# Kernel tuning notes

Hardware: AMD Instinct MI355X
Metric: run time of the kernel (lower is better)

The kernel has to match this reference:

```python
import jax, jax.numpy as jnp
import numpy as np
from jax.scipy.stats import norm as jnorm

B, S, D, H, E, K, FF = 8, 256, 1024, 16, 4, 2, 4096
HD = D // H
NOISE_EPS = 0.01
LOSS_COEF = 0.01
EPS_FILL = float(np.finfo(float).eps)


def _ln(x, g, b):
    m = x.mean(-1, keepdims=True)
    v = x.var(-1, keepdims=True)
    return (x - m) * jax.lax.rsqrt(v + 1e-5) * g + b


def setup_inputs() -> dict:
    key = jax.random.key(0)
    ks = jax.random.split(key, 16)
    r = lambda i, shape, s=1.0: jax.random.normal(ks[i], shape, dtype=jnp.float32) * s
    return {
        "x": r(0, (B, S, D)),
        "e_outputs": r(1, (B, 64, D)),            # unused (is_lm=True) but part of signature
        "noise": r(2, (B, E)),                     # the randn_like(clean_logits) draw
        "w_gate": r(3, (D, E), 0.02),
        "w_noise": r(4, (D, E), 0.02),
        "Wq": r(5, (E, D, D), 0.02),
        "Wk": r(6, (E, D, D), 0.02),
        "Wv": r(7, (E, D, D), 0.02),
        "Wo": r(8, (E, D, D), 0.02),
        "W1": r(9, (E, D, FF), 0.02),
        "b1": jnp.zeros((E, FF), jnp.float32),
        "W2": r(10, (E, FF, D), 0.02),
        "b2": jnp.zeros((E, D), jnp.float32),
        "g1": jnp.ones((E, D), jnp.float32),
        "be1": jnp.zeros((E, D), jnp.float32),
        "g2": jnp.ones((E, D), jnp.float32),
        "be2": jnp.zeros((E, D), jnp.float32),
        "trg_mask": jnp.tril(jnp.ones((S, S), dtype=bool))[None, None],  # causal [1,1,S,S]
        "src_mask": jnp.ones((1, 1, 1, 64), dtype=bool),                 # unused (is_lm=True)
    }


def _cv_squared(v):
    # torch .var() is unbiased (ddof=1)
    return v.var(ddof=1) / (v.mean() ** 2 + 1e-10)


def reference(x, e_outputs, noise, w_gate, w_noise, Wq, Wk, Wv, Wo, W1, b1, W2, b2,
              g1, be1, g2, be2, trg_mask, src_mask):
    b, s, d = x.shape
    # ---- noisy top-k gating (per sample, on the sequence-sum) ----
    xs = x.sum(axis=1)                                   # [B, D]
    clean = xs @ w_gate                                  # [B, E]
    raw_noise = xs @ w_noise                             # [B, E]
    stddev = jax.nn.softplus(raw_noise) + NOISE_EPS      # train=True -> *1.0
    noisy = clean + noise * stddev                       # logits
    top_logits, top_idx = jax.lax.top_k(noisy, K + 1)    # [B, K+1]
    topk_gates = jax.nn.softmax(top_logits[:, :K], axis=1)
    gates = jnp.zeros_like(noisy).at[jnp.arange(b)[:, None], top_idx[:, :K]].set(topk_gates)
    # load: prob each expert's clean logit lands in the noisy top-k
    thr_in = top_logits[:, K:K + 1]                      # (k+1)-th noisy value
    thr_out = top_logits[:, K - 1:K]                     # k-th noisy value
    is_in = noisy > thr_in
    prob = jnp.where(is_in,
                     jnorm.cdf((clean - thr_in) / stddev),
                     jnorm.cdf((clean - thr_out) / stddev))
    load = prob.sum(0)                                   # [E]
    importance = gates.sum(0)                            # [E]
    loss = (_cv_squared(importance) + _cv_squared(load)) * LOSS_COEF

    # ---- experts: standard decoder layer (self-attn + FFN), is_lm -> no cross-attn ----
    neg = jnp.asarray(-1e9, x.dtype)
    scale = 1.0 / np.sqrt(HD)

    def expert(p):
        wq, wk, wv, wo, w1, bb1, w2, bb2, gg1, bbe1, gg2, bbe2 = p
        q = (x @ wq).reshape(b, s, H, HD)
        k_ = (x @ wk).reshape(b, s, H, HD)
        v = (x @ wv).reshape(b, s, H, HD)
        scores = jnp.einsum('bqhd,bkhd->bhqk', q, k_) * scale
        scores = jnp.where(trg_mask, scores, neg)
        attn = jax.nn.softmax(scores, axis=-1)
        o = jnp.einsum('bhqk,bkhd->bqhd', attn, v).reshape(b, s, d) @ wo
        h = _ln(x + o, gg1, bbe1)
        ff = jax.nn.relu(h @ w1 + bb1) @ w2 + bb2
        return _ln(h + ff, gg2, bbe2)

    outs = jax.vmap(expert)((Wq, Wk, Wv, Wo, W1, b1, W2, b2, g1, be1, g2, be2))  # [E,B,S,D]

    # ---- combine: scatter-add of gate-weighted expert outputs (dense equivalent) ----
    y = jnp.einsum('be,ebsd->bsd', gates, outs)
    y = jnp.where(y == 0, jnp.asarray(EPS_FILL, y.dtype), y)
    return y, loss
```

## Files before the change

### kernel.cpp

```cpp
#include <hip/hip_runtime.h>
#include <hip/hip_bf16.h>

typedef __bf16 bf16;
typedef __attribute__((ext_vector_type(4))) __bf16 bf16x4;
typedef __attribute__((ext_vector_type(8))) __bf16 bf16x8;
typedef __attribute__((ext_vector_type(4))) float floatx4;

constexpr int CB = 8, CS = 256, CD = 1024, CH = 16, CE = 4, CFF = 4096, CHD = 64;
constexpr long long DD  = 1048576;
constexpr long long DFF = 4194304;
constexpr long long BSD = 2097152;
constexpr long long PSD = 4194304;

constexpr size_t OFF_PART = 0;
constexpr size_t OFF_CLEAN= 262144;
constexpr size_t OFF_RAW  = 262272;
constexpr size_t OFF_GATES= 262400;
constexpr size_t OFF_EACT = 262528;
constexpr size_t OFF_PBE  = 262592;
constexpr size_t OFF_BP   = 262656;
constexpr size_t OFF_XBF  = 263168;
constexpr size_t OFF_WT   = OFF_XBF + (size_t)BSD*2;
constexpr size_t OFF_W1T  = OFF_WT  + (size_t)16*DD*2;
constexpr size_t OFF_W2T  = OFF_W1T + (size_t)4*DFF*2;
constexpr size_t OFF_QKV  = OFF_W2T + (size_t)4*DFF*2;
constexpr size_t OFF_AO   = OFF_QKV + (size_t)3*PSD*2;
constexpr size_t OFF_F1   = OFF_QKV;
constexpr size_t OFF_PB   = OFF_AO  + (size_t)PSD*2;
constexpr size_t OFF_VT   = OFF_PB;
constexpr size_t OFF_H    = OFF_PB  + (size_t)2*PSD*4;
constexpr size_t OFF_HBF  = OFF_H   + (size_t)PSD*4;

__global__ __launch_bounds__(256)
void wtrans_cvt(const float* __restrict__ Wq, const float* __restrict__ Wk,
                const float* __restrict__ Wv, const float* __restrict__ Wo,
                const float* __restrict__ W1, const float* __restrict__ W2,
                bf16* __restrict__ wT, bf16* __restrict__ w1T, bf16* __restrict__ w2T,
                const float* __restrict__ x, bf16* __restrict__ xbf, float* __restrict__ part) {
  int zb = blockIdx.x;
  if (zb >= 3072) {
    int blk = zb - 3072;
    int b = blk >> 3, ch = blk & 7;
    int t = threadIdx.x;
    float s0 = 0.f, s1 = 0.f, s2 = 0.f, s3 = 0.f;
    long long base4 = ((long long)(b*CS + ch*32))*CD / 4;
#pragma unroll 4
    for (int r = 0; r < 32; ++r) {
      long long i4 = base4 + (long long)r*(CD/4) + t;
      float4 v = ((const float4*)x)[i4];
      bf16x4 o; o[0] = (bf16)v.x; o[1] = (bf16)v.y; o[2] = (bf16)v.z; o[3] = (bf16)v.w;
      ((bf16x4*)xbf)[i4] = o;
      s0 += v.x; s1 += v.y; s2 += v.z; s3 += v.w;
    }
    float4 sv; sv.x = s0; sv.y = s1; sv.z = s2; sv.w = s3;
    ((float4*)(part + (long long)blk*CD))[t] = sv;
    return;
  }
  int w = threadIdx.x >> 6;
  const float* src; bf16* d; int rows, cols, btk, btn;
  if (zb < 1024) {
    int m = zb >> 6, bt = zb & 63; int e = m >> 2; int which = m & 3;
    src = ((which == 0) ? Wq : (which == 1) ? Wk : (which == 2) ? Wv : Wo) + (long long)e*DD;
    d = wT + (long long)m*DD; rows = 1024; cols = 1024;
    btk = bt >> 3; btn = bt & 7;
  } else if (zb < 2048) {
    int z2 = zb - 1024; int e = z2 >> 8; int bt = z2 & 255;
    src = W1 + (long long)e*DFF; d = w1T + (long long)e*DFF;
    rows = 1024; cols = 4096; btk = bt >> 5; btn = bt & 31;
  } else {
    int z3 = zb - 2048; int e = z3 >> 8; int bt = z3 & 255;
    src = W2 + (long long)e*DFF; d = w2T + (long long)e*DFF;
    rows = 4096; cols = 1024; btk = bt >> 3; btn = bt & 7;
  }
  int tk = btk*2 + (w & 1);
  int tn = btn*2 + (w >> 1);
  int lane = threadIdx.x & 63;
  int ln = lane >> 3, lk = lane & 7;
  int k0 = tk*64, n0 = tn*64;
  const float* s = src + (long long)(k0 + lk*8)*cols + n0 + ln*8;
  floatx4 f[8][2];
#pragma unroll
  for (int j = 0; j < 8; ++j) {
    f[j][0] = __builtin_nontemporal_load((const floatx4*)(s + (long long)j*cols));
    f[j][1] = __builtin_nontemporal_load((const floatx4*)(s + (long long)j*cols + 4));
  }
  bf16* dp = d + (long long)(n0 + ln*8)*rows + k0 + lk*8;
#pragma unroll
  for (int jn = 0; jn < 8; ++jn) {
    bf16x8 o;
#pragma unroll
    for (int jk = 0; jk < 8; ++jk) {
      o[jk] = (bf16)f[jk][jn >> 2][jn & 3];
    }
    *(bf16x8*)(dp + (long long)jn*rows) = o;
  }
}

__global__ __launch_bounds__(256)
void gate_fused(const float* __restrict__ part, const float* __restrict__ wg,
                const float* __restrict__ wn, const float* __restrict__ noise,
                float* __restrict__ gates, int* __restrict__ eact, int* __restrict__ pairBE,
                int* __restrict__ batchPair, float* __restrict__ loss_out) {
  int t = threadIdx.x;
  float4 wgv[4], wnv[4];
  float xv[CB][4];
#pragma unroll
  for (int k = 0; k < 4; ++k) {
    int d = t + k*256;
    wgv[k] = ((const float4*)wg)[d];
    wnv[k] = ((const float4*)wn)[d];
#pragma unroll
    for (int b = 0; b < CB; ++b) {
      float s = 0.f;
#pragma unroll
      for (int c = 0; c < 8; ++c) s += part[(long long)(b*8 + c)*CD + d];
      xv[b][k] = s;
    }
  }
  __shared__ float red[4][64];
  __shared__ float sCR[64];
  int lane = t & 63, wv = t >> 6;
#pragma unroll
  for (int b = 0; b < CB; ++b) {
#pragma unroll
    for (int e = 0; e < CE; ++e) {
      float s1 = 0.f, s2 = 0.f;
#pragma unroll
      for (int k = 0; k < 4; ++k) {
        const float* g  = (const float*)&wgv[k];
        const float* nn = (const float*)&wnv[k];
        s1 += xv[b][k]*g[e];
        s2 += xv[b][k]*nn[e];
      }
      for (int off = 32; off; off >>= 1) { s1 += __shfl_xor(s1, off); s2 += __shfl_xor(s2, off); }
      if (lane == 0) { red[wv][b*4 + e] = s1; red[wv][32 + b*4 + e] = s2; }
    }
  }
  __syncthreads();
  if (t < 64) sCR[t] = red[0][t] + red[1][t] + red[2][t] + red[3][t];
  __syncthreads();
  if (t != 0) return;
  const float* clean = sCR;
  const float* raw   = sCR + 32;
  float imp[CE] = {0,0,0,0}, load[CE] = {0,0,0,0};
  int act[CE] = {0,0,0,0};
  for (int b = 0; b < CB; ++b) {
    float cl[CE], sd[CE], ny[CE];
    for (int e = 0; e < CE; ++e) {
      cl[e] = clean[b*CE + e];
      float rw = raw[b*CE + e];
      float sp = fmaxf(rw, 0.f) + log1pf(expf(-fabsf(rw)));
      sd[e] = sp + 0.01f;
      ny[e] = cl[e] + noise[b*CE + e]*sd[e];
    }
    int idx[CE] = {0,1,2,3};
    for (int a = 0; a < 3; ++a) {
      int best = a;
      for (int c = a + 1; c < 4; ++c) if (ny[idx[c]] > ny[idx[best]]) best = c;
      int tt = idx[a]; idx[a] = idx[best]; idx[best] = tt;
    }
    float l0 = ny[idx[0]], l1 = ny[idx[1]], l2 = ny[idx[2]];
    float e1 = expf(l1 - l0);
    float g0 = 1.f/(1.f + e1), g1v = e1/(1.f + e1);
    for (int e = 0; e < CE; ++e) gates[b*CE + e] = 0.f;
    gates[b*CE + idx[0]] = g0; gates[b*CE + idx[1]] = g1v;
    imp[idx[0]] += g0; imp[idx[1]] += g1v;
    act[idx[0]] = 1; act[idx[1]] = 1;
    for (int e = 0; e < CE; ++e) {
      bool is_in = ny[e] > l2;
      float thr = is_in ? l2 : l1;
      float zz = (cl[e] - thr) / sd[e];
      load[e] += 0.5f * erfcf(-zz * 0.70710678118654752440f);
    }
  }
  int pe2p[CB][CE];
  int pc = 0;
  for (int e = 0; e < CE; ++e)
    for (int b = 0; b < CB; ++b)
      if (gates[b*CE + e] != 0.f) { pairBE[pc] = b | (e << 8); pe2p[b][e] = pc; ++pc; }
  for (int b = 0; b < CB; ++b) {
    int s = 0;
    for (int e = 0; e < CE; ++e)
      if (gates[b*CE + e] != 0.f) batchPair[2*b + (s++)] = pe2p[b][e];
  }
  float m1 = 0.f, m2 = 0.f;
  for (int e = 0; e < CE; ++e) { m1 += imp[e]; m2 += load[e]; }
  m1 *= 0.25f; m2 *= 0.25f;
  float v1 = 0.f, v2 = 0.f;
  for (int e = 0; e < CE; ++e) { float d1 = imp[e]-m1, d2 = load[e]-m2; v1 += d1*d1; v2 += d2*d2; }
  v1 *= (1.f/3.f); v2 *= (1.f/3.f);
  loss_out[0] = 0.01f * (v1/(m1*m1 + 1e-10f) + v2/(m2*m2 + 1e-10f));
  for (int e = 0; e < CE; ++e) eact[e] = act[e];
}

__global__ __launch_bounds__(256)
void transpose_v(const bf16* __restrict__ qkvC, bf16* __restrict__ vTb) {
  int z = blockIdx.x; int p = z >> 4, h = z & 15;
  int w = threadIdx.x >> 6, lane = threadIdx.x & 63;
  int ln = lane >> 3, lk = lane & 7;
  const bf16* v = qkvC + 2*PSD + ((long long)(p*CS + w*64 + ln*8))*CD + h*CHD + lk*8;
  bf16x8 in[8];
#pragma unroll
  for (int j = 0; j < 8; ++j) in[j] = *(const bf16x8*)(v + (long long)j*CD);
  bf16* vt = vTb + ((long long)(p*CH + h)*CHD + lk*8)*CS + w*64 + ln*8;
#pragma unroll
  for (int dn = 0; dn < 8; ++dn) {
    bf16x8 o;
#pragma unroll
    for (int j = 0; j < 8; ++j) o[j] = in[j][dn];
    *(bf16x8*)(vt + (long long)dn*CS) = o;
  }
}

__device__ __forceinline__ void cp16(const bf16* g, bf16* l) {
  __builtin_amdgcn_global_load_lds((const __attribute__((address_space(1))) void*)g,
                                   (__attribute__((address_space(3))) void*)l, 16, 0, 0);
}

template<int R, int W, int NT>
__device__ __forceinline__ void stageN(const bf16* __restrict__ src, int ld, bf16* dst) {
  constexpr int W8 = W/8;
  int t = threadIdx.x;
  int l = t & 63, wid = t >> 6;
#pragma unroll
  for (int i = 0; i < (R*W8)/NT; ++i) {
    int idb = i*NT + wid*64;
    int id = idb + l;
    int row = id / W8, sl = id % W8;
    int gc = sl ^ (row & 7);
    cp16(src + (long long)row*ld + gc*8, dst + (long long)idb*8);
  }
}

__global__ __launch_bounds__(256)
void attn_fused(const bf16* __restrict__ qkvC, const bf16* __restrict__ vTb,
                bf16* __restrict__ aoC) {
  int h = blockIdx.x, p = blockIdx.y, qt = blockIdx.z;
  const bf16* qp = qkvC + (long long)(p*CS)*CD + h*CHD;
  const bf16* kp = qp + PSD;
  const bf16* vt = vTb + (long long)(p*CH + h)*CHD*CS;
  bf16* aop = aoC + (long long)(p*CS)*CD + h*CHD;

  __shared__ bf16 Ps[64*264];
  __shared__ float smaxL[64*4], ssumL[64*4], Lrow[64];

  int t = threadIdx.x, w = t >> 6, lane = t & 63, lr = lane & 15, quad = lane >> 4;

  floatx4 accs[4][4] = {};
  if (w <= qt) {
#pragma unroll
    for (int kk = 0; kk < 2; ++kk) {
      int c = kk*4 + quad;
      bf16x8 af[4], bfr[4];
#pragma unroll
      for (int i = 0; i < 4; ++i) {
        af[i]  = *(const bf16x8*)(qp + (long long)(qt*64 + i*16 + lr)*CD + c*8);
        bfr[i] = *(const bf16x8*)(kp + (long long)(w*64  + i*16 + lr)*CD + c*8);
      }
#pragma unroll
      for (int i = 0; i < 4; ++i)
#pragma unroll
        for (int j = 0; j < 4; ++j)
          accs[i][j] = __builtin_amdgcn_mfma_f32_16x16x32_bf16(af[i], bfr[j], accs[i][j], 0, 0, 0);
    }
  }
  float rmax[4][4];
#pragma unroll
  for (int i = 0; i < 4; ++i)
#pragma unroll
    for (int r = 0; r < 4; ++r) {
      int qrow = qt*64 + i*16 + quad*4 + r;
      float m = -3.0e38f;
#pragma unroll
      for (int j = 0; j < 4; ++j) {
        int kcol = w*64 + j*16 + lr;
        float s = accs[i][j][r]*0.125f;
        s = (kcol <= qrow) ? s : -3.0e38f;
        accs[i][j][r] = s;
        m = fmaxf(m, s);
      }
      rmax[i][r] = m;
    }
#pragma unroll
  for (int off = 1; off <= 8; off <<= 1)
#pragma unroll
    for (int i = 0; i < 4; ++i)
#pragma unroll
      for (int r = 0; r < 4; ++r) rmax[i][r] = fmaxf(rmax[i][r], __shfl_xor(rmax[i][r], off));
  if (lr == 0)
#pragma unroll
    for (int i = 0; i < 4; ++i)
#pragma unroll
      for (int r = 0; r < 4; ++r) smaxL[(i*16 + quad*4 + r)*4 + w] = rmax[i][r];
  __syncthreads();
  float rsum[4][4];
#pragma unroll
  for (int i = 0; i < 4; ++i)
#pragma unroll
    for (int r = 0; r < 4; ++r) {
      floatx4 mv = *(const floatx4*)&smaxL[(i*16 + quad*4 + r)*4];
      float M = fmaxf(fmaxf(mv[0], mv[1]), fmaxf(mv[2], mv[3]));
      float srow = 0.f;
#pragma unroll
      for (int j = 0; j < 4; ++j) {
        float pp = __expf(accs[i][j][r] - M);
        accs[i][j][r] = pp;
        srow += pp;
      }
      rsum[i][r] = srow;
    }
#pragma unroll
  for (int off = 1; off <= 8; off <<= 1)
#pragma unroll
    for (int i = 0; i < 4; ++i)
#pragma unroll
      for (int r = 0; r < 4; ++r) rsum[i][r] += __shfl_xor(rsum[i][r], off);
  if (lr == 0)
#pragma unroll
    for (int i = 0; i < 4; ++i)
#pragma unroll
      for (int r = 0; r < 4; ++r) ssumL[(i*16 + quad*4 + r)*4 + w] = rsum[i][r];
  __syncthreads();
  if (w == 0 && lr == 0) {
#pragma unroll
    for (int i = 0; i < 4; ++i)
#pragma unroll
      for (int r = 0; r < 4; ++r) {
        int m = i*16 + quad*4 + r;
        floatx4 sv = *(const floatx4*)&ssumL[m*4];
        Lrow[m] = sv[0] + sv[1] + sv[2] + sv[3];
      }
  }
  if (w <= qt) {
#pragma unroll
    for (int i = 0; i < 4; ++i)
#pragma unroll
      for (int j = 0; j < 4; ++j)
#pragma unroll
        for (int r = 0; r < 4; ++r)
          Ps[(i*16 + quad*4 + r)*264 + w*64 + j*16 + lr] = (bf16)accs[i][j][r];
  }
  __syncthreads();
  floatx4 acco[4] = {};
  int ksMax = (qt + 1)*2;
  for (int ks = 0; ks < ksMax; ++ks) {
    int c = ks*4 + quad;
    bf16x8 ap = *(const bf16x8*)(Ps + (w*16 + lr)*264 + c*8);
#pragma unroll
    for (int j = 0; j < 4; ++j) {
      bf16x8 bv = *(const bf16x8*)(vt + (long long)(j*16 + lr)*CS + c*8);
      acco[j] = __builtin_amdgcn_mfma_f32_16x16x32_bf16(ap, bv, acco[j], 0, 0, 0);
    }
  }
#pragma unroll
  for (int r = 0; r < 4; ++r) {
    int orow = w*16 + quad*4 + r;
    float inv = 1.f / Lrow[orow];
#pragma unroll
    for (int j = 0; j < 4; ++j)
      aop[(long long)(qt*64 + orow)*CD + j*16 + lr] = (bf16)(acco[j][r]*inv);
  }
}

__global__ __launch_bounds__(256)
void ln1_kernel(const float* __restrict__ x, const float* __restrict__ PbF,
                const float* __restrict__ gamma, const float* __restrict__ beta,
                float* __restrict__ h, bf16* __restrict__ hbf, const int* __restrict__ pairBE) {
  int row = blockIdx.x;
  int pbe = pairBE[row >> 8]; int pb = pbe & 255, pe = pbe >> 8;
  int t = threadIdx.x;
  float4 a = ((const float4*)(x + ((long long)pb*CS + (row & 255))*CD))[t];
  float4 b = ((const float4*)(PbF + (long long)row*CD))[t];
  float4 c = ((const float4*)(PbF + PSD + (long long)row*CD))[t];
  float v0 = a.x + b.x + c.x, v1 = a.y + b.y + c.y;
  float v2 = a.z + b.z + c.z, v3 = a.w + b.w + c.w;
  float s  = v0 + v1 + v2 + v3;
  float s2 = v0*v0 + v1*v1 + v2*v2 + v3*v3;
  int lane = t & 63, wave = t >> 6;
  for (int off = 32; off; off >>= 1) { s += __shfl_xor(s, off); s2 += __shfl_xor(s2, off); }
  __shared__ float red[8];
  if (lane == 0) { red[wave*2] = s; red[wave*2 + 1] = s2; }
  __syncthreads();
  s  = red[0] + red[2] + red[4] + red[6];
  s2 = red[1] + red[3] + red[5] + red[7];
  float mean = s * (1.f/CD);
  float rstd = rsqrtf(s2*(1.f/CD) - mean*mean + 1e-5f);
  float4 gm = ((const float4*)(gamma + (long long)pe*CD))[t];
  float4 bt = ((const float4*)(beta  + (long long)pe*CD))[t];
  float4 o;
  o.x = (v0 - mean)*rstd*gm.x + bt.x;
  o.y = (v1 - mean)*rstd*gm.y + bt.y;
  o.z = (v2 - mean)*rstd*gm.z + bt.z;
  o.w = (v3 - mean)*rstd*gm.w + bt.w;
  ((float4*)(h + (long long)row*CD))[t] = o;
  bf16x4 ob; ob[0] = (bf16)o.x; ob[1] = (bf16)o.y; ob[2] = (bf16)o.z; ob[3] = (bf16)o.w;
  ((bf16x4*)(hbf + (long long)row*CD))[t] = ob;
}

__global__ __launch_bounds__(256)
void ln2y_kernel(const float* __restrict__ h, const bf16* __restrict__ PbB,
                 const float* __restrict__ gamma, const float* __restrict__ beta,
                 float* __restrict__ y, const float* __restrict__ gates,
                 const int* __restrict__ pairBE, const int* __restrict__ batchPair) {
  int row = blockIdx.x;
  int b = row >> 8, sIdx = row & 255;
  int p0 = batchPair[2*b], p1 = batchPair[2*b + 1];
  int e0 = pairBE[p0] >> 8, e1 = pairBE[p1] >> 8;
  float gv0 = gates[b*CE + e0], gv1 = gates[b*CE + e1];
  long long r0 = (long long)p0*CS + sIdx, r1 = (long long)p1*CS + sIdx;
  int t = threadIdx.x;
  float4 a = ((const float4*)(h + r0*CD))[t];
  float4 c = ((const float4*)(h + r1*CD))[t];
#pragma unroll
  for (int k = 0; k < 4; ++k) {
    bf16x4 pa = ((const bf16x4*)(PbB + (long long)k*PSD + r0*CD))[t];
    bf16x4 pc = ((const bf16x4*)(PbB + (long long)k*PSD + r1*CD))[t];
    a.x += (float)pa[0]; a.y += (float)pa[1]; a.z += (float)pa[2]; a.w += (float)pa[3];
    c.x += (float)pc[0]; c.y += (float)pc[1]; c.z += (float)pc[2]; c.w += (float)pc[3];
  }
  float sA = a.x + a.y + a.z + a.w;
  float sA2 = a.x*a.x + a.y*a.y + a.z*a.z + a.w*a.w;
  float sB = c.x + c.y + c.z + c.w;
  float sB2 = c.x*c.x + c.y*c.y + c.z*c.z + c.w*c.w;
  int lane = t & 63, wave = t >> 6;
  for (int off = 32; off; off >>= 1) {
    sA += __shfl_xor(sA, off); sA2 += __shfl_xor(sA2, off);
    sB += __shfl_xor(sB, off); sB2 += __shfl_xor(sB2, off);
  }
  __shared__ float red[16];
  if (lane == 0) { red[wave*4] = sA; red[wave*4+1] = sA2; red[wave*4+2] = sB; red[wave*4+3] = sB2; }
  __syncthreads();
  sA  = red[0] + red[4] + red[8]  + red[12];
  sA2 = red[1] + red[5] + red[9]  + red[13];
  sB  = red[2] + red[6] + red[10] + red[14];
  sB2 = red[3] + red[7] + red[11] + red[15];
  float mA = sA*(1.f/CD), mB = sB*(1.f/CD);
  float rsA = rsqrtf(sA2*(1.f/CD) - mA*mA + 1e-5f);
  float rsB = rsqrtf(sB2*(1.f/CD) - mB*mB + 1e-5f);
  float4 gm0 = ((const float4*)(gamma + (long long)e0*CD))[t];
  float4 bt0 = ((const float4*)(beta  + (long long)e0*CD))[t];
  float4 gm1 = ((const float4*)(gamma + (long long)e1*CD))[t];
  float4 bt1 = ((const float4*)(beta  + (long long)e1*CD))[t];
  float4 o;
  o.x = gv0*((a.x - mA)*rsA*gm0.x + bt0.x) + gv1*((c.x - mB)*rsB*gm1.x + bt1.x);
  o.y = gv0*((a.y - mA)*rsA*gm0.y + bt0.y) + gv1*((c.y - mB)*rsB*gm1.y + bt1.y);
  o.z = gv0*((a.z - mA)*rsA*gm0.z + bt0.z) + gv1*((c.z - mB)*rsB*gm1.z + bt1.z);
  o.w = gv0*((a.w - mA)*rsA*gm0.w + bt0.w) + gv1*((c.w - mB)*rsB*gm1.w + bt1.w);
  constexpr float EF = 2.2204460492503131e-16f;
  o.x = (o.x == 0.f) ? EF : o.x;  o.y = (o.y == 0.f) ? EF : o.y;
  o.z = (o.z == 0.f) ? EF : o.z;  o.w = (o.w == 0.f) ? EF : o.w;
  ((float4*)(y + (long long)row*CD))[t] = o;
}

enum { EPI_BF16 = 0, EPI_F32 = 1, EPI_BRELU = 2, EPI_BIASBF16 = 3 };

template<int EPI, int KS, bool A_BATCH, int BM>
__global__ __launch_bounds__(512, 2)
void gemm_nt(const bf16* __restrict__ A, const bf16* __restrict__ Bt, void* __restrict__ Cv,
             int K , int lda, int ldb, int ldc,
             long long oBe, long long oBmat, long long oCmat, long long oCk,
             const float* __restrict__ bias, long long biasStride,
             const int* __restrict__ pairBE) {
  constexpr int BN = 256;
  constexpr int NBUF = (BM == 128) ? 3 : 2;
  constexpr int DEPTH = NBUF - 1;
  constexpr int MI = BM / 32;
  int z = blockIdx.z;
  int zk = z % KS, mat = z / KS;
  int gx = gridDim.x;
  int nwg = gx * gridDim.y;
  int lin = blockIdx.x + gx*blockIdx.y;
  int nl  = (lin & 7)*(nwg >> 3) + (lin >> 3);
  int m0 = (nl % gx) * BM, n0 = (nl / gx) * BN;
  int pbe = pairBE[m0 >> 8]; int pb = pbe & 255, pe = pbe >> 8;
  const bf16* Ab = A + (A_BATCH ? ((long long)pb*CS + (m0 & 255))*lda : (long long)m0*lda)
                     + (long long)zk*K;
  const bf16* Bb = Bt + (long long)pe*oBe + (long long)mat*oBmat + (long long)zk*K
                      + (long long)n0*ldb;
  long long coff = (long long)mat*oCmat + (long long)zk*oCk;

  __shared__ bf16 As[NBUF][BM*64];
  __shared__ bf16 Bs[NBUF][BN*64];

  int wave = threadIdx.x >> 6;
  int lane = threadIdx.x & 63;
  int wm = wave >> 2, wn = wave & 3;
  int lr = lane & 15;
  int quad = lane >> 4;

  floatx4 acc[MI][4] = {};

  int nt = K / 64;
#pragma unroll
  for (int d = 0; d < DEPTH; ++d) {
    stageN<BM, 64, 512>(Ab + d*64, lda, As[d]);
    stageN<BN, 64, 512>(Bb + d*64, ldb, Bs[d]);
  }
  int cur = 0, stg = DEPTH;
  for (int t = 0; t < nt; ++t) {
    if (t + DEPTH < nt) {
      stageN<BM, 64, 512>(Ab + (t+DEPTH)*64, lda, As[stg]);
      stageN<BN, 64, 512>(Bb + (t+DEPTH)*64, ldb, Bs[stg]);
      if (++stg == NBUF) stg = 0;
      if constexpr (BM == 128) asm volatile("s_waitcnt vmcnt(12)" ::: "memory");
      else                     asm volatile("s_waitcnt vmcnt(8)"  ::: "memory");
    } else if (t + 1 < nt) {
      if constexpr (BM == 128) asm volatile("s_waitcnt vmcnt(6)"  ::: "memory");
      else                     asm volatile("s_waitcnt vmcnt(0)"  ::: "memory");
    } else {
      asm volatile("s_waitcnt vmcnt(0)" ::: "memory");
    }
    __builtin_amdgcn_s_barrier();
    asm volatile("" ::: "memory");
#pragma unroll
    for (int kk = 0; kk < 2; ++kk) {
      int c = kk*4 + quad;
      bf16x8 af[MI], bfr[4];
#pragma unroll
      for (int i = 0; i < MI; ++i) {
        int m = wm*(BM/2) + i*16 + lr;
        af[i] = *(const bf16x8*)(As[cur] + m*64 + ((c ^ (m & 7))*8));
      }
#pragma unroll
      for (int j = 0; j < 4; ++j) {
        int n = wn*64 + j*16 + lr;
        bfr[j] = *(const bf16x8*)(Bs[cur] + n*64 + ((c ^ (n & 7))*8));
      }
#pragma unroll
      for (int i = 0; i < MI; ++i)
#pragma unroll
        for (int j = 0; j < 4; ++j)
          acc[i][j] = __builtin_amdgcn_mfma_f32_16x16x32_bf16(af[i], bfr[j], acc[i][j], 0, 0, 0);
    }
    if (++cur == NBUF) cur = 0;
    __builtin_amdgcn_s_barrier();
    asm volatile("" ::: "memory");
  }

#pragma unroll
  for (int j = 0; j < 4; ++j) {
    int col = n0 + wn*64 + j*16 + lr;
    float bv = 0.f;
    if constexpr (EPI == EPI_BRELU || EPI == EPI_BIASBF16)
      if (zk == 0) bv = bias[(long long)pe*biasStride + col];
#pragma unroll
    for (int i = 0; i < MI; ++i) {
#pragma unroll
      for (int r = 0; r < 4; ++r) {
        int row = m0 + wm*(BM/2) + i*16 + quad*4 + r;
        float v = acc[i][j][r] + bv;
        long long idx = coff + (long long)row*ldc + col;
        if constexpr (EPI == EPI_BF16)          ((bf16*)Cv)[idx] = (bf16)v;
        else if constexpr (EPI == EPI_F32)      ((float*)Cv)[idx] = v;
        else if constexpr (EPI == EPI_BRELU)    ((bf16*)Cv)[idx] = (bf16)fmaxf(v, 0.f);
        else                                    ((bf16*)Cv)[idx] = (bf16)v;
      }
    }
  }
}

extern "C" void kernel_launch(void* const* d_in, const int* in_sizes, int n_in,
                              void* d_out, int out_size, void* d_ws, size_t ws_size,
                              hipStream_t stream) {
  const float* x       = (const float*)d_in[0];
  const float* noise   = (const float*)d_in[2];
  const float* w_gate  = (const float*)d_in[3];
  const float* w_noise = (const float*)d_in[4];
  const float* Wq      = (const float*)d_in[5];
  const float* Wk      = (const float*)d_in[6];
  const float* Wv      = (const float*)d_in[7];
  const float* Wo      = (const float*)d_in[8];
  const float* W1      = (const float*)d_in[9];
  const float* b1      = (const float*)d_in[10];
  const float* W2      = (const float*)d_in[11];
  const float* b2      = (const float*)d_in[12];
  const float* g1      = (const float*)d_in[13];
  const float* be1     = (const float*)d_in[14];
  const float* g2      = (const float*)d_in[15];
  const float* be2     = (const float*)d_in[16];

  char* ws = (char*)d_ws;
  float* y    = (float*)d_out;
  float* loss = y + (size_t)BSD;

  float* part  = (float*)(ws + OFF_PART);
  float* gates = (float*)(ws + OFF_GATES);
  int*   eact  = (int*)  (ws + OFF_EACT);
  int*   pairBE= (int*)  (ws + OFF_PBE);
  int*   batchPair = (int*)(ws + OFF_BP);
  bf16*  xbf   = (bf16*) (ws + OFF_XBF);
  bf16*  wT    = (bf16*) (ws + OFF_WT);
  bf16*  w1T   = (bf16*) (ws + OFF_W1T);
  bf16*  w2T   = (bf16*) (ws + OFF_W2T);
  bf16*  qkvC  = (bf16*) (ws + OFF_QKV);
  bf16*  aoC   = (bf16*) (ws + OFF_AO);
  bf16*  f1    = (bf16*) (ws + OFF_F1);
  bf16*  vTb   = (bf16*) (ws + OFF_VT);
  float* PbF   = (float*)(ws + OFF_PB);
  bf16*  PbB   = (bf16*) (ws + OFF_PB);
  float* h     = (float*)(ws + OFF_H);
  bf16*  hbf   = (bf16*) (ws + OFF_HBF);

  wtrans_cvt<<<3136, 256, 0, stream>>>(Wq, Wk, Wv, Wo, W1, W2, wT, w1T, w2T, x, xbf, part);
  gate_fused<<<1, 256, 0, stream>>>(part, w_gate, w_noise, noise, gates, eact, pairBE, batchPair, loss);

  gemm_nt<EPI_BF16, 1, true, 128><<<dim3(32, 4, 3), 512, 0, stream>>>(
      xbf, wT, qkvC, 1024, 1024, 1024, 1024,
      4*DD, DD, PSD, 0, nullptr, 0, pairBE);

  transpose_v<<<256, 256, 0, stream>>>(qkvC, vTb);

  attn_fused<<<dim3(CH, 16, 4), 256, 0, stream>>>(qkvC, vTb, aoC);

  gemm_nt<EPI_F32, 2, false, 128><<<dim3(32, 4, 2), 512, 0, stream>>>(
      aoC, wT + 3*DD, PbF, 512, 1024, 1024, 1024,
      4*DD, 0, 0, PSD, nullptr, 0, pairBE);

  ln1_kernel<<<4096, 256, 0, stream>>>(x, PbF, g1, be1, h, hbf, pairBE);

  gemm_nt<EPI_BRELU, 1, false, 256><<<dim3(16, 16, 1), 512, 0, stream>>>(
      hbf, w1T, f1, 1024, 1024, 1024, 4096,
      DFF, 0, 0, 0, b1, CFF, pairBE);

  gemm_nt<EPI_BIASBF16, 4, false, 256><<<dim3(16, 4, 4), 512, 0, stream>>>(
      f1, w2T, PbB, 1024, 4096, 4096, 1024,
      DFF, 0, 0, PSD, b2, CD, pairBE);

  ln2y_kernel<<<2048, 256, 0, stream>>>(h, PbB, g2, be2, y, gates, pairBE, batchPair);
}
```

Measured before the change: 496.4 us.

## Overlap W1/W2 weight transpose with attention and revert GEMM to fixed 256 tiles

The W1/W2 fp32-to-bf16 transpose blocks move out of the first prep kernel and into the attention launch as extra blocks. The attention grid is flattened, with the largest causal query tiles scheduled first. The goal is to hide the weight-conversion traffic behind the compute-bound attention phase. The GEMM template also drops its BM=128 triple-buffered variant, so every GEMM now uses 256x256 tiles with double buffering. That halves the grid for the QKV and output-projection GEMMs and may reduce occupancy or pipelining depth on those launches.

Result: no change. 490.7 us (-1.1%).

```diff
diff --git a/kernel.cpp b/kernel.cpp
--- a/kernel.cpp
+++ b/kernel.cpp
@@ -13,8 +13,6 @@
 constexpr long long PSD = 4194304;
 
 constexpr size_t OFF_PART = 0;
-constexpr size_t OFF_CLEAN= 262144;
-constexpr size_t OFF_RAW  = 262272;
 constexpr size_t OFF_GATES= 262400;
 constexpr size_t OFF_EACT = 262528;
 constexpr size_t OFF_PBE  = 262592;
@@ -31,15 +29,41 @@
 constexpr size_t OFF_H    = OFF_PB  + (size_t)2*PSD*4;
 constexpr size_t OFF_HBF  = OFF_H   + (size_t)PSD*4;
 
+__device__ __forceinline__ void wtile_trans(const float* __restrict__ src, bf16* __restrict__ d,
+                                            int rows, int cols, int btk, int btn) {
+  int w = threadIdx.x >> 6;
+  int tk = btk*2 + (w & 1);
+  int tn = btn*2 + (w >> 1);
+  int lane = threadIdx.x & 63;
+  int ln = lane >> 3, lk = lane & 7;
+  int k0 = tk*64, n0 = tn*64;
+  const float* s = src + (long long)(k0 + lk*8)*cols + n0 + ln*8;
+  floatx4 f[8][2];
+#pragma unroll
+  for (int j = 0; j < 8; ++j) {
+    f[j][0] = __builtin_nontemporal_load((const floatx4*)(s + (long long)j*cols));
+    f[j][1] = __builtin_nontemporal_load((const floatx4*)(s + (long long)j*cols + 4));
+  }
+  bf16* dp = d + (long long)(n0 + ln*8)*rows + k0 + lk*8;
+#pragma unroll
+  for (int jn = 0; jn < 8; ++jn) {
+    bf16x8 o;
+#pragma unroll
+    for (int jk = 0; jk < 8; ++jk) {
+      o[jk] = (bf16)f[jk][jn >> 2][jn & 3];
+    }
+    *(bf16x8*)(dp + (long long)jn*rows) = o;
+  }
+}
+
 __global__ __launch_bounds__(256)
 void wtrans_cvt(const float* __restrict__ Wq, const float* __restrict__ Wk,
                 const float* __restrict__ Wv, const float* __restrict__ Wo,
-                const float* __restrict__ W1, const float* __restrict__ W2,
-                bf16* __restrict__ wT, bf16* __restrict__ w1T, bf16* __restrict__ w2T,
+                bf16* __restrict__ wT,
                 const float* __restrict__ x, bf16* __restrict__ xbf, float* __restrict__ part) {
   int zb = blockIdx.x;
-  if (zb >= 3072) {
-    int blk = zb - 3072;
+  if (zb >= 1024) {
+    int blk = zb - 1024;
     int b = blk >> 3, ch = blk & 7;
     int t = threadIdx.x;
     float s0 = 0.f, s1 = 0.f, s2 = 0.f, s3 = 0.f;
@@ -56,44 +80,11 @@
     ((float4*)(part + (long long)blk*CD))[t] = sv;
     return;
   }
-  int w = threadIdx.x >> 6;
-  const float* src; bf16* d; int rows, cols, btk, btn;
-  if (zb < 1024) {
-    int m = zb >> 6, bt = zb & 63; int e = m >> 2; int which = m & 3;
-    src = ((which == 0) ? Wq : (which == 1) ? Wk : (which == 2) ? Wv : Wo) + (long long)e*DD;
-    d = wT + (long long)m*DD; rows = 1024; cols = 1024;
-    btk = bt >> 3; btn = bt & 7;
-  } else if (zb < 2048) {
-    int z2 = zb - 1024; int e = z2 >> 8; int bt = z2 & 255;
-    src = W1 + (long long)e*DFF; d = w1T + (long long)e*DFF;
-    rows = 1024; cols = 4096; btk = bt >> 5; btn = bt & 31;
-  } else {
-    int z3 = zb - 2048; int e = z3 >> 8; int bt = z3 & 255;
-    src = W2 + (long long)e*DFF; d = w2T + (long long)e*DFF;
-    rows = 4096; cols = 1024; btk = bt >> 3; btn = bt & 7;
-  }
-  int tk = btk*2 + (w & 1);
-  int tn = btn*2 + (w >> 1);
-  int lane = threadIdx.x & 63;
-  int ln = lane >> 3, lk = lane & 7;
-  int k0 = tk*64, n0 = tn*64;
-  const float* s = src + (long long)(k0 + lk*8)*cols + n0 + ln*8;
-  floatx4 f[8][2];
-#pragma unroll
-  for (int j = 0; j < 8; ++j) {
-    f[j][0] = __builtin_nontemporal_load((const floatx4*)(s + (long long)j*cols));
-    f[j][1] = __builtin_nontemporal_load((const floatx4*)(s + (long long)j*cols + 4));
-  }
-  bf16* dp = d + (long long)(n0 + ln*8)*rows + k0 + lk*8;
-#pragma unroll
-  for (int jn = 0; jn < 8; ++jn) {
-    bf16x8 o;
-#pragma unroll
-    for (int jk = 0; jk < 8; ++jk) {
-      o[jk] = (bf16)f[jk][jn >> 2][jn & 3];
-    }
-    *(bf16x8*)(dp + (long long)jn*rows) = o;
-  }
+  int m = zb >> 6, bt = zb & 63; int e = m >> 2; int which = m & 3;
+  const float* src = ((which == 0) ? Wq : (which == 1) ? Wk : (which == 2) ? Wv : Wo)
+                     + (long long)e*DD;
+  bf16* d = wT + (long long)m*DD;
+  wtile_trans(src, d, 1024, 1024, bt >> 3, bt & 7);
 }
 
 __global__ __launch_bounds__(256)
@@ -233,9 +224,27 @@
 }
 
 __global__ __launch_bounds__(256)
-void attn_fused(const bf16* __restrict__ qkvC, const bf16* __restrict__ vTb,
-                bf16* __restrict__ aoC) {
-  int h = blockIdx.x, p = blockIdx.y, qt = blockIdx.z;
+void attn_wtrans(const bf16* __restrict__ qkvC, const bf16* __restrict__ vTb,
+                 bf16* __restrict__ aoC,
+                 const float* __restrict__ W1, const float* __restrict__ W2,
+                 bf16* __restrict__ w1T, bf16* __restrict__ w2T) {
+  int z = blockIdx.x;
+  if (z >= 1024) {
+    int zt = z - 1024;
+    const float* src; bf16* d; int rows, cols, btk, btn;
+    if (zt < 1024) {
+      int e = zt >> 8; int bt = zt & 255;
+      src = W1 + (long long)e*DFF; d = w1T + (long long)e*DFF;
+      rows = 1024; cols = 4096; btk = bt >> 5; btn = bt & 31;
+    } else {
+      int z3 = zt - 1024; int e = z3 >> 8; int bt = z3 & 255;
+      src = W2 + (long long)e*DFF; d = w2T + (long long)e*DFF;
+      rows = 4096; cols = 1024; btk = bt >> 3; btn = bt & 7;
+    }
+    wtile_trans(src, d, rows, cols, btk, btn);
+    return;
+  }
+  int h = z & 15, p = (z >> 4) & 15, qt = 3 - (z >> 8);
   const bf16* qp = qkvC + (long long)(p*CS)*CD + h*CHD;
   const bf16* kp = qp + PSD;
   const bf16* vt = vTb + (long long)(p*CH + h)*CHD*CS;
@@ -454,17 +463,14 @@
 
 enum { EPI_BF16 = 0, EPI_F32 = 1, EPI_BRELU = 2, EPI_BIASBF16 = 3 };
 
-template<int EPI, int KS, bool A_BATCH, int BM>
+template<int EPI, int KS, bool A_BATCH>
 __global__ __launch_bounds__(512, 2)
 void gemm_nt(const bf16* __restrict__ A, const bf16* __restrict__ Bt, void* __restrict__ Cv,
              int K , int lda, int ldb, int ldc,
              long long oBe, long long oBmat, long long oCmat, long long oCk,
              const float* __restrict__ bias, long long biasStride,
              const int* __restrict__ pairBE) {
-  constexpr int BN = 256;
-  constexpr int NBUF = (BM == 128) ? 3 : 2;
-  constexpr int DEPTH = NBUF - 1;
-  constexpr int MI = BM / 32;
+  constexpr int BM = 256, BN = 256;
   int z = blockIdx.z;
   int zk = z % KS, mat = z / KS;
   int gx = gridDim.x;
@@ -479,8 +485,8 @@
                       + (long long)n0*ldb;
   long long coff = (long long)mat*oCmat + (long long)zk*oCk;
 
-  __shared__ bf16 As[NBUF][BM*64];
-  __shared__ bf16 Bs[NBUF][BN*64];
+  __shared__ bf16 As[2][BM*64];
+  __shared__ bf16 Bs[2][BN*64];
 
   int wave = threadIdx.x >> 6;
   int lane = threadIdx.x & 63;
@@ -488,25 +494,17 @@
   int lr = lane & 15;
   int quad = lane >> 4;
 
-  floatx4 acc[MI][4] = {};
+  floatx4 acc[8][4] = {};
 
   int nt = K / 64;
-#pragma unroll
-  for (int d = 0; d < DEPTH; ++d) {
-    stageN<BM, 64, 512>(Ab + d*64, lda, As[d]);
-    stageN<BN, 64, 512>(Bb + d*64, ldb, Bs[d]);
-  }
-  int cur = 0, stg = DEPTH;
+  stageN<BM, 64, 512>(Ab, lda, As[0]);
+  stageN<BN, 64, 512>(Bb, ldb, Bs[0]);
   for (int t = 0; t < nt; ++t) {
-    if (t + DEPTH < nt) {
-      stageN<BM, 64, 512>(Ab + (t+DEPTH)*64, lda, As[stg]);
-      stageN<BN, 64, 512>(Bb + (t+DEPTH)*64, ldb, Bs[stg]);
-      if (++stg == NBUF) stg = 0;
-      if constexpr (BM == 128) asm volatile("s_waitcnt vmcnt(12)" ::: "memory");
-      else                     asm volatile("s_waitcnt vmcnt(8)"  ::: "memory");
-    } else if (t + 1 < nt) {
-      if constexpr (BM == 128) asm volatile("s_waitcnt vmcnt(6)"  ::: "memory");
-      else                     asm volatile("s_waitcnt vmcnt(0)"  ::: "memory");
+    int cur = t & 1;
+    if (t + 1 < nt) {
+      stageN<BM, 64, 512>(Ab + (t+1)*64, lda, As[cur ^ 1]);
+      stageN<BN, 64, 512>(Bb + (t+1)*64, ldb, Bs[cur ^ 1]);
+      asm volatile("s_waitcnt vmcnt(8)" ::: "memory");
     } else {
       asm volatile("s_waitcnt vmcnt(0)" ::: "memory");
     }
@@ -515,10 +513,10 @@
 #pragma unroll
     for (int kk = 0; kk < 2; ++kk) {
       int c = kk*4 + quad;
-      bf16x8 af[MI], bfr[4];
-#pragma unroll
-      for (int i = 0; i < MI; ++i) {
-        int m = wm*(BM/2) + i*16 + lr;
+      bf16x8 af[8], bfr[4];
+#pragma unroll
+      for (int i = 0; i < 8; ++i) {
+        int m = wm*128 + i*16 + lr;
         af[i] = *(const bf16x8*)(As[cur] + m*64 + ((c ^ (m & 7))*8));
       }
 #pragma unroll
@@ -527,12 +525,11 @@
         bfr[j] = *(const bf16x8*)(Bs[cur] + n*64 + ((c ^ (n & 7))*8));
       }
 #pragma unroll
-      for (int i = 0; i < MI; ++i)
+      for (int i = 0; i < 8; ++i)
 #pragma unroll
         for (int j = 0; j < 4; ++j)
           acc[i][j] = __builtin_amdgcn_mfma_f32_16x16x32_bf16(af[i], bfr[j], acc[i][j], 0, 0, 0);
     }
-    if (++cur == NBUF) cur = 0;
     __builtin_amdgcn_s_barrier();
     asm volatile("" ::: "memory");
   }
@@ -544,10 +541,10 @@
     if constexpr (EPI == EPI_BRELU || EPI == EPI_BIASBF16)
       if (zk == 0) bv = bias[(long long)pe*biasStride + col];
 #pragma unroll
-    for (int i = 0; i < MI; ++i) {
+    for (int i = 0; i < 8; ++i) {
 #pragma unroll
       for (int r = 0; r < 4; ++r) {
-        int row = m0 + wm*(BM/2) + i*16 + quad*4 + r;
+        int row = m0 + wm*128 + i*16 + quad*4 + r;
         float v = acc[i][j][r] + bv;
         long long idx = coff + (long long)row*ldc + col;
         if constexpr (EPI == EPI_BF16)          ((bf16*)Cv)[idx] = (bf16)v;
@@ -601,28 +598,28 @@
   float* h     = (float*)(ws + OFF_H);
   bf16*  hbf   = (bf16*) (ws + OFF_HBF);
 
-  wtrans_cvt<<<3136, 256, 0, stream>>>(Wq, Wk, Wv, Wo, W1, W2, wT, w1T, w2T, x, xbf, part);
+  wtrans_cvt<<<1088, 256, 0, stream>>>(Wq, Wk, Wv, Wo, wT, x, xbf, part);
   gate_fused<<<1, 256, 0, stream>>>(part, w_gate, w_noise, noise, gates, eact, pairBE, batchPair, loss);
 
-  gemm_nt<EPI_BF16, 1, true, 128><<<dim3(32, 4, 3), 512, 0, stream>>>(
+  gemm_nt<EPI_BF16, 1, true><<<dim3(16, 4, 3), 512, 0, stream>>>(
       xbf, wT, qkvC, 1024, 1024, 1024, 1024,
       4*DD, DD, PSD, 0, nullptr, 0, pairBE);
 
   transpose_v<<<256, 256, 0, stream>>>(qkvC, vTb);
 
-  attn_fused<<<dim3(CH, 16, 4), 256, 0, stream>>>(qkvC, vTb, aoC);
-
-  gemm_nt<EPI_F32, 2, false, 128><<<dim3(32, 4, 2), 512, 0, stream>>>(
+  attn_wtrans<<<3072, 256, 0, stream>>>(qkvC, vTb, aoC, W1, W2, w1T, w2T);
+
+  gemm_nt<EPI_F32, 2, false><<<dim3(16, 4, 2), 512, 0, stream>>>(
       aoC, wT + 3*DD, PbF, 512, 1024, 1024, 1024,
       4*DD, 0, 0, PSD, nullptr, 0, pairBE);
 
   ln1_kernel<<<4096, 256, 0, stream>>>(x, PbF, g1, be1, h, hbf, pairBE);
 
-  gemm_nt<EPI_BRELU, 1, false, 256><<<dim3(16, 16, 1), 512, 0, stream>>>(
+  gemm_nt<EPI_BRELU, 1, false><<<dim3(16, 16, 1), 512, 0, stream>>>(
       hbf, w1T, f1, 1024, 1024, 1024, 4096,
       DFF, 0, 0, 0, b1, CFF, pairBE);
 
-  gemm_nt<EPI_BIASBF16, 4, false, 256><<<dim3(16, 4, 4), 512, 0, stream>>>(
+  gemm_nt<EPI_BIASBF16, 4, false><<<dim3(16, 4, 4), 512, 0, stream>>>(
       f1, w2T, PbB, 1024, 4096, 4096, 1024,
       DFF, 0, 0, PSD, b2, CD, pairBE);
 
```
